# Optimization experiments

Hardware: AMD Instinct MI355X
Metric: run time of the kernel (lower is better)

The kernel has to match this reference:

```python
import jax, jax.numpy as jnp
import numpy as np

IN_C, OUT_C = 128, 256
KH, KW = 3, 3
STRIDE = (1, 1)
PAD = (1, 1)


def setup_inputs() -> dict:
    key = jax.random.key(0)
    kx, kw = jax.random.split(key)
    x = jax.random.normal(kx, (32, IN_C, 56, 56), dtype=jnp.float32)
    k = 1.0 / (IN_C * KH * KW)
    weight = (2.0 * jax.random.uniform(kw, (OUT_C, IN_C, KH, KW), dtype=jnp.float32) - 1.0) * (k ** 0.5)
    return {"x": x, "weight": weight}


def reference(x, weight):
    # Equivalent to the as_strided broadcast-multiply-sum: a plain 2D cross-correlation
    # (no bias), NCHW input, OIHW weight, stride (1,1), padding (1,1).
    return jax.lax.conv_general_dilated(
        x, weight,
        window_strides=STRIDE,
        padding=[(PAD[0], PAD[0]), (PAD[1], PAD[1])],
        dimension_numbers=("NCHW", "OIHW", "NCHW"),
    )
```

## Files before the change

kernel.cpp:

```cpp
#include <hip/hip_runtime.h>

typedef __attribute__((ext_vector_type(8))) short short8;
typedef __attribute__((ext_vector_type(4))) float floatx4;

#define IN_C 128
#define OUT_C 256
#define NB 32
#define HW 56
#define S_PER_N (HW * HW)
#define M_TOTAL (NB * S_PER_N)
#define PH 58
#define PW 66
#define XN_ELEMS (NB * PH * PW * IN_C)
#define WT_ELEMS (9 * OUT_C * IN_C)

__device__ __forceinline__ unsigned short f2bf(float f) {
    unsigned int u = __builtin_bit_cast(unsigned int, f);
    u = (u + 0x7FFFu + ((u >> 16) & 1u)) >> 16;
    return (unsigned short)u;
}

__device__ __forceinline__ void gld_lds16(const unsigned short* g, unsigned short* l) {
    __builtin_amdgcn_global_load_lds(
        (const __attribute__((address_space(1))) unsigned int*)g,
        (__attribute__((address_space(3))) unsigned int*)l, 16, 0, 0);
}

__global__ void xform_x(const float* __restrict__ x, unsigned short* __restrict__ xn) {
    const int ihp = blockIdx.x;
    const int n   = blockIdx.y;
    const int tid = threadIdx.x;
    unsigned int* __restrict__ row32 =
        (unsigned int*)(xn + (size_t)(n * PH + ihp) * PW * IN_C);
    const int WORDS = PW * IN_C / 2;

    if (ihp == 0 || ihp == PH - 1) {
        for (int i = tid; i < WORDS; i += 256) row32[i] = 0u;
        return;
    }
    const int ih = ihp - 1;
    __shared__ unsigned short lds2[HW][IN_C];
    const float* __restrict__ xrow = x + (size_t)n * IN_C * S_PER_N + (size_t)ih * HW;
    for (int i = tid; i < IN_C * 14; i += 256) {
        int ic = i / 14, iw4 = (i % 14) * 4;
        float4 v = *(const float4*)(xrow + (size_t)ic * S_PER_N + iw4);
        lds2[iw4 + 0][ic] = f2bf(v.x);
        lds2[iw4 + 1][ic] = f2bf(v.y);
        lds2[iw4 + 2][ic] = f2bf(v.z);
        lds2[iw4 + 3][ic] = f2bf(v.w);
    }
    __syncthreads();
    for (int wi = tid; wi < WORDS; wi += 256) {
        int pix = wi >> 6;
        int icw = wi & 63;
        unsigned int val = 0u;
        if (pix >= 1 && pix <= HW)
            val = *(const unsigned int*)&lds2[pix - 1][icw * 2];
        row32[wi] = val;
    }
}

__global__ void xform_w(const float* __restrict__ w, unsigned short* __restrict__ wt) {
    const int idx = blockIdx.x * 256 + threadIdx.x;
    const int ic  = idx & 127;
    const int oc  = (idx >> 7) & 255;
    const int khw = idx >> 15;
    wt[idx] = f2bf(w[(oc * IN_C + ic) * 9 + khw]);
}

__global__ void __launch_bounds__(256, 3)
conv_mfma(const unsigned short* __restrict__ xn,
          const unsigned short* __restrict__ wt,
          float* __restrict__ out) {
    const int tid  = threadIdx.x;
    const int lane = tid & 63;
    const int wv   = tid >> 6;
    const int l15  = lane & 15;
    const int quad = lane >> 4;

    const int bx0 = blockIdx.x;
    const int bx  = (bx0 & 7) * 196 + (bx0 >> 3);
    const int tile_oc = bx & 1;
    const int tile_m  = bx >> 1;

    const int s_blk  = tile_m * 128;
    const int oc_blk = tile_oc * 128;
    const int s0  = s_blk + (wv & 1) * 64;
    const int oc0 = oc_blk + (wv >> 1) * 64;

    __shared__ unsigned short A_lds[128 * 64];
    __shared__ unsigned short B_lds[128 * 64];

    const int srow = tid >> 3;
    const int sic  = ((tid & 7) ^ (srow & 7)) * 8;

    const unsigned short* a_g[4];
    const unsigned short* b_g[4];
#pragma unroll
    for (int q = 0; q < 4; ++q) {
        int row = q * 32 + srow;
        a_g[q] = wt + (size_t)(oc_blk + row) * IN_C + sic;
        int sg = s_blk + row;
        int n  = sg / S_PER_N;
        int r  = sg % S_PER_N;
        int oh = r / HW, ow = r % HW;
        b_g[q] = xn + (size_t)((n * PH + oh) * PW + ow) * IN_C + sic;
    }
    unsigned short* a_l = A_lds + tid * 8;
    unsigned short* b_l = B_lds + tid * 8;

    const int fr7 = l15 & 7;
    int afo[4], bfo[4];
#pragma unroll
    for (int i = 0; i < 4; ++i)
        afo[i] = ((wv >> 1) * 64 + i * 16 + l15) * 64 + ((quad ^ fr7) * 8);
#pragma unroll
    for (int j = 0; j < 4; ++j)
        bfo[j] = ((wv & 1) * 64 + j * 16 + l15) * 64 + ((quad ^ fr7) * 8);

    floatx4 acc[4][4];
#pragma unroll
    for (int i = 0; i < 4; ++i)
#pragma unroll
        for (int j = 0; j < 4; ++j) acc[i][j] = (floatx4){0.f, 0.f, 0.f, 0.f};

#pragma unroll
    for (int khw = 0; khw < 9; ++khw) {
        const int xo = ((khw / 3) * PW + (khw % 3)) * IN_C;
        const int wo = khw * OUT_C * IN_C;
#pragma unroll
        for (int h = 0; h < 2; ++h) {
            const int ic0 = h * 64;
            __syncthreads();
#pragma unroll
            for (int q = 0; q < 4; ++q) {
                gld_lds16(a_g[q] + wo + ic0, a_l + q * 2048);
                gld_lds16(b_g[q] + xo + ic0, b_l + q * 2048);
            }
            __syncthreads();

#pragma unroll
            for (int kk = 0; kk < 2; ++kk) {
                const int ko = kk * 32;
                short8 a[4], b[4];
#pragma unroll
                for (int i = 0; i < 4; ++i) a[i] = *(const short8*)(A_lds + (afo[i] ^ ko));
#pragma unroll
                for (int j = 0; j < 4; ++j) b[j] = *(const short8*)(B_lds + (bfo[j] ^ ko));
#pragma unroll
                for (int i = 0; i < 4; ++i)
#pragma unroll
                    for (int j = 0; j < 4; ++j)
                        acc[i][j] = __builtin_amdgcn_mfma_f32_16x16x32_bf16(
                            a[i], b[j], acc[i][j], 0, 0, 0);
            }
        }
    }

#pragma unroll
    for (int j = 0; j < 4; ++j) {
        int s_glob = s0 + j * 16 + l15;
        int n = s_glob / S_PER_N;
        int s = s_glob % S_PER_N;
        float* obase = out + (size_t)n * OUT_C * S_PER_N + s;
#pragma unroll
        for (int i = 0; i < 4; ++i) {
            int oc = oc0 + i * 16 + quad * 4;
#pragma unroll
            for (int r = 0; r < 4; ++r)
                obase[(size_t)(oc + r) * S_PER_N] = acc[i][j][r];
        }
    }
}

extern "C" void kernel_launch(void* const* d_in, const int* in_sizes, int n_in,
                              void* d_out, int out_size, void* d_ws, size_t ws_size,
                              hipStream_t stream) {
    const float* x = (const float*)d_in[0];
    const float* w = (const float*)d_in[1];
    float* out = (float*)d_out;

    unsigned short* xn = (unsigned short*)d_ws;
    unsigned short* wt = xn + XN_ELEMS;

    dim3 gx(PH, NB);
    xform_x<<<gx, 256, 0, stream>>>(x, xn);
    xform_w<<<WT_ELEMS / 256, 256, 0, stream>>>(w, wt);
    conv_mfma<<<(M_TOTAL / 128) * 2, 256, 0, stream>>>(xn, wt, out);
}
```

Measured before the change: 205.2 us.

## Enlarge conv tile to 256x256 with double-buffered LDS prefetch

Each block now covers all 256 output channels for 256 spatial positions, using 512 threads with eight waves. The K-loop double-buffers LDS so the next 64-channel slice is fetched while the current one is computed, and MFMA issue is bracketed with s_setprio. The larger tile is meant to raise data reuse and hide global-load latency behind compute. In exchange it uses 128KB of LDS and 128 accumulator registers per lane, which lowers occupancy, and it adds extra barriers inside each slice.

```diff
diff --git a/kernel.cpp b/kernel.cpp
--- a/kernel.cpp
+++ b/kernel.cpp
@@ -68,28 +68,25 @@
     wt[idx] = f2bf(w[(oc * IN_C + ic) * 9 + khw]);
 }
 
-__global__ void __launch_bounds__(256, 3)
+__global__ void __launch_bounds__(512, 2)
 conv_mfma(const unsigned short* __restrict__ xn,
           const unsigned short* __restrict__ wt,
           float* __restrict__ out) {
     const int tid  = threadIdx.x;
     const int lane = tid & 63;
     const int wv   = tid >> 6;
+    const int wm   = wv >> 2;
+    const int wn   = wv & 3;
     const int l15  = lane & 15;
     const int quad = lane >> 4;
-
-    const int bx0 = blockIdx.x;
-    const int bx  = (bx0 & 7) * 196 + (bx0 >> 3);
-    const int tile_oc = bx & 1;
-    const int tile_m  = bx >> 1;
-
-    const int s_blk  = tile_m * 128;
-    const int oc_blk = tile_oc * 128;
-    const int s0  = s_blk + (wv & 1) * 64;
-    const int oc0 = oc_blk + (wv >> 1) * 64;
-
-    __shared__ unsigned short A_lds[128 * 64];
-    __shared__ unsigned short B_lds[128 * 64];
+    const int fr7  = l15 & 7;
+
+    const int bx0    = blockIdx.x;
+    const int tile_m = (bx0 & 7) * 49 + (bx0 >> 3);
+    const int s_blk  = tile_m * 256;
+
+    __shared__ unsigned short A_lds[2][256 * 64];
+    __shared__ unsigned short B_lds[2][256 * 64];
 
     const int srow = tid >> 3;
     const int sic  = ((tid & 7) ^ (srow & 7)) * 8;
@@ -97,66 +94,92 @@
     const unsigned short* a_g[4];
     const unsigned short* b_g[4];
 #pragma unroll
-    for (int q = 0; q < 4; ++q) {
-        int row = q * 32 + srow;
-        a_g[q] = wt + (size_t)(oc_blk + row) * IN_C + sic;
+    for (int g = 0; g < 4; ++g) {
+        int row = g * 64 + srow;
+        a_g[g] = wt + (size_t)row * IN_C + sic;
         int sg = s_blk + row;
         int n  = sg / S_PER_N;
-        int r  = sg % S_PER_N;
-        int oh = r / HW, ow = r % HW;
-        b_g[q] = xn + (size_t)((n * PH + oh) * PW + ow) * IN_C + sic;
-    }
-    unsigned short* a_l = A_lds + tid * 8;
-    unsigned short* b_l = B_lds + tid * 8;
-
-    const int fr7 = l15 & 7;
-    int afo[4], bfo[4];
-#pragma unroll
-    for (int i = 0; i < 4; ++i)
-        afo[i] = ((wv >> 1) * 64 + i * 16 + l15) * 64 + ((quad ^ fr7) * 8);
-#pragma unroll
-    for (int j = 0; j < 4; ++j)
-        bfo[j] = ((wv & 1) * 64 + j * 16 + l15) * 64 + ((quad ^ fr7) * 8);
-
-    floatx4 acc[4][4];
-#pragma unroll
-    for (int i = 0; i < 4; ++i)
+        int r2 = sg % S_PER_N;
+        int oh = r2 / HW, ow = r2 % HW;
+        b_g[g] = xn + (size_t)((n * PH + oh) * PW + ow) * IN_C + sic;
+    }
+
+    const int slot = (quad ^ fr7) * 8;
+    int a_base[2], b_base[2];
+#pragma unroll
+    for (int kk = 0; kk < 2; ++kk) {
+        a_base[kk] = (wm * 128 + l15) * 64 + (slot ^ (kk * 32));
+        b_base[kk] = (wn * 64  + l15) * 64 + (slot ^ (kk * 32));
+    }
+
+    floatx4 acc[8][4];
+#pragma unroll
+    for (int i = 0; i < 8; ++i)
 #pragma unroll
         for (int j = 0; j < 4; ++j) acc[i][j] = (floatx4){0.f, 0.f, 0.f, 0.f};
 
 #pragma unroll
+    for (int g = 0; g < 4; ++g) {
+        gld_lds16(a_g[g], &A_lds[0][g * 4096 + tid * 8]);
+        gld_lds16(b_g[g], &B_lds[0][g * 4096 + tid * 8]);
+    }
+    asm volatile("s_waitcnt vmcnt(0)" ::: "memory");
+    __builtin_amdgcn_s_barrier();
+
+    int xo = 0;
+#pragma unroll 1
     for (int khw = 0; khw < 9; ++khw) {
-        const int xo = ((khw / 3) * PW + (khw % 3)) * IN_C;
-        const int wo = khw * OUT_C * IN_C;
+        const int wo  = khw * (OUT_C * IN_C);
+        const int kwv = khw - (khw / 3) * 3;
+        const int xo_next = (kwv == 2) ? (xo + (PW - 2) * IN_C) : (xo + IN_C);
 #pragma unroll
         for (int h = 0; h < 2; ++h) {
-            const int ic0 = h * 64;
-            __syncthreads();
+            if (khw < 8 || h == 0) {
+                const int awo = (h == 0) ? (wo + 64) : (wo + OUT_C * IN_C);
+                const int bxo = (h == 0) ? (xo + 64) : xo_next;
+#pragma unroll
+                for (int g = 0; g < 4; ++g) {
+                    gld_lds16(a_g[g] + awo, &A_lds[1 - h][g * 4096 + tid * 8]);
+                    gld_lds16(b_g[g] + bxo, &B_lds[1 - h][g * 4096 + tid * 8]);
+                }
+            }
+            const unsigned short* Ab = &A_lds[h][0];
+            const unsigned short* Bb = &B_lds[h][0];
 #pragma unroll
             for (int q = 0; q < 4; ++q) {
-                gld_lds16(a_g[q] + wo + ic0, a_l + q * 2048);
-                gld_lds16(b_g[q] + xo + ic0, b_l + q * 2048);
+                const int mh = q >> 1, nh = q & 1;
+                short8 a[4][2], b[2][2];
+#pragma unroll
+                for (int kk = 0; kk < 2; ++kk) {
+#pragma unroll
+                    for (int ii = 0; ii < 4; ++ii)
+                        a[ii][kk] = *(const short8*)(Ab + a_base[kk] + (mh * 4 + ii) * 1024);
+#pragma unroll
+                    for (int jj = 0; jj < 2; ++jj)
+                        b[jj][kk] = *(const short8*)(Bb + b_base[kk] + (nh * 2 + jj) * 1024);
+                }
+                __builtin_amdgcn_s_setprio(1);
+#pragma unroll
+                for (int kk = 0; kk < 2; ++kk)
+#pragma unroll
+                    for (int ii = 0; ii < 4; ++ii)
+#pragma unroll
+                        for (int jj = 0; jj < 2; ++jj)
+                            acc[mh * 4 + ii][nh * 2 + jj] =
+                                __builtin_amdgcn_mfma_f32_16x16x32_bf16(
+                                    a[ii][kk], b[jj][kk],
+                                    acc[mh * 4 + ii][nh * 2 + jj], 0, 0, 0);
+                __builtin_amdgcn_s_setprio(0);
+                __builtin_amdgcn_s_barrier();
             }
-            __syncthreads();
-
-#pragma unroll
-            for (int kk = 0; kk < 2; ++kk) {
-                const int ko = kk * 32;
-                short8 a[4], b[4];
-#pragma unroll
-                for (int i = 0; i < 4; ++i) a[i] = *(const short8*)(A_lds + (afo[i] ^ ko));
-#pragma unroll
-                for (int j = 0; j < 4; ++j) b[j] = *(const short8*)(B_lds + (bfo[j] ^ ko));
-#pragma unroll
-                for (int i = 0; i < 4; ++i)
-#pragma unroll
-                    for (int j = 0; j < 4; ++j)
-                        acc[i][j] = __builtin_amdgcn_mfma_f32_16x16x32_bf16(
-                            a[i], b[j], acc[i][j], 0, 0, 0);
-            }
+            asm volatile("s_waitcnt vmcnt(0)" ::: "memory");
+            __builtin_amdgcn_s_barrier();
         }
-    }
-
+        xo = xo_next;
+    }
+
+    const int s0  = s_blk + wn * 64;
+    const int oc0 = wm * 128;
 #pragma unroll
     for (int j = 0; j < 4; ++j) {
         int s_glob = s0 + j * 16 + l15;
@@ -164,7 +187,7 @@
         int s = s_glob % S_PER_N;
         float* obase = out + (size_t)n * OUT_C * S_PER_N + s;
 #pragma unroll
-        for (int i = 0; i < 4; ++i) {
+        for (int i = 0; i < 8; ++i) {
             int oc = oc0 + i * 16 + quad * 4;
 #pragma unroll
             for (int r = 0; r < 4; ++r)
@@ -186,5 +209,5 @@
     dim3 gx(PH, NB);
     xform_x<<<gx, 256, 0, stream>>>(x, xn);
     xform_w<<<WT_ELEMS / 256, 256, 0, stream>>>(w, wt);
-    conv_mfma<<<(M_TOTAL / 128) * 2, 256, 0, stream>>>(xn, wt, out);
-}
+    conv_mfma<<<M_TOTAL / 256, 512, 0, stream>>>(xn, wt, out);
+}
```

Result: slower. 223.8 us (+9.1%).
